# Performance work log

Measured on AMD Instinct MI355X. Metric: run time of the kernel, lower is better.

Reference implementation:

```python
import jax, jax.numpy as jnp
import numpy as np


def spiral_cw(H, W):
    idx = []
    top, bottom, left, right = 0, H - 1, 0, W - 1
    while top <= bottom and left <= right:
        for j in range(left, right + 1):
            idx.append((top, j))
        top += 1
        for i in range(top, bottom + 1):
            idx.append((i, right))
        right -= 1
        if top <= bottom:
            for j in range(right, left - 1, -1):
                idx.append((bottom, j))
            bottom -= 1
        if left <= right:
            for i in range(bottom, top - 1, -1):
                idx.append((i, left))
            left += 1
    return [i * W + j for i, j in idx]


def spiral_ccw(H, W):
    idx = []
    top, bottom, left, right = 0, H - 1, 0, W - 1
    while top <= bottom and left <= right:
        for j in range(right, left - 1, -1):
            idx.append((top, j))
        top += 1
        for i in range(top, bottom + 1):
            idx.append((i, left))
        left += 1
        if top <= bottom:
            for j in range(left, right + 1):
                idx.append((bottom, j))
            bottom -= 1
        if left <= right:
            for i in range(bottom, top - 1, -1):
                idx.append((i, right))
            right -= 1
    return [i * W + j for i, j in idx]


def silu(x):
    return x * jax.nn.sigmoid(x)


def mamba_fwd(x, in_w, conv_w, conv_b, xproj_w, dtp_w, dtp_b, A_log, D, out_w):
    # x: [B,L,dm]; expand=1 so d_inner == dm
    B, L, dm = x.shape
    d_inner = in_w.shape[1] // 2
    N = A_log.shape[1]          # d_state = 16
    K = conv_w.shape[1]         # d_conv = 4
    xz = x @ in_w               # [B,L,2*d_inner]
    u, z = jnp.split(xz, 2, axis=-1)
    # causal depthwise conv over L (kernel K), then SiLU
    up = jnp.pad(u, ((0, 0), (K - 1, 0), (0, 0)))
    uc = conv_b + sum(conv_w[:, k] * up[:, k:k + L, :] for k in range(K))
    uc = silu(uc)
    dbl = uc @ xproj_w          # [B,L,dt_rank+2N]
    dt_rank = dbl.shape[-1] - 2 * N
    dtc = dbl[..., :dt_rank]
    Bv = dbl[..., dt_rank:dt_rank + N]
    Cv = dbl[..., dt_rank + N:]
    dt = jax.nn.softplus(dtc @ dtp_w + dtp_b)   # [B,L,d_inner]
    A = -jnp.exp(A_log)                          # [d_inner,N]
    dA = jnp.exp(dt[..., None] * A)              # [B,L,d_inner,N]
    dBu = dt[..., None] * Bv[:, :, None, :] * uc[..., None]

    def step(h, inp):
        dA_t, dBu_t = inp
        h = h * dA_t + dBu_t
        return h, h

    h0 = jnp.zeros((B, d_inner, N), x.dtype)
    _, hs = jax.lax.scan(step, h0, (jnp.moveaxis(dA, 1, 0), jnp.moveaxis(dBu, 1, 0)))
    hs = jnp.moveaxis(hs, 0, 1)                  # [B,L,d_inner,N]
    y = jnp.einsum('bldn,bln->bld', hs, Cv) + D * uc
    y = y * silu(z)
    return y @ out_w


def setup_inputs():
    key = jax.random.key(0)
    ks = jax.random.split(key, 32)
    B, Hh, Ww, C = 4, 32, 32, 768
    L = Hh * Ww
    N, dr, K = 16, 48, 4

    def p(i, shape, s=0.02):
        return jax.random.normal(ks[i], shape, jnp.float32) * s

    d = {}
    d['x'] = jax.random.normal(ks[0], (B, L, C), jnp.float32)
    d['norm_w'] = jnp.ones((C,), jnp.float32)
    d['norm_b'] = jnp.zeros((C,), jnp.float32)
    for i, pre in enumerate(['cw', 'ccw']):
        o = 1 + i * 8
        d[pre + '_in_w'] = p(o, (C, 2 * C))
        d[pre + '_conv_w'] = p(o + 1, (C, K), 0.2)
        d[pre + '_conv_b'] = jnp.zeros((C,), jnp.float32)
        d[pre + '_xproj_w'] = p(o + 2, (C, dr + 2 * N))
        d[pre + '_dtp_w'] = p(o + 3, (dr, C), 0.1)
        d[pre + '_dtp_b'] = jnp.full((C,), -4.0, jnp.float32) + p(o + 4, (C,), 0.5)
        d[pre + '_A_log'] = jnp.log(jnp.broadcast_to(jnp.arange(1, N + 1, dtype=jnp.float32), (C, N)))
        d[pre + '_D'] = jnp.ones((C,), jnp.float32)
        d[pre + '_out_w'] = p(o + 5, (C, C))
    d['fus_w1'] = p(20, (2 * C, C))
    d['fus_b1'] = jnp.zeros((C,), jnp.float32)
    d['fus_w2'] = p(21, (C, C))
    d['fus_b2'] = jnp.zeros((C,), jnp.float32)
    return d


def reference(x, norm_w, norm_b,
              cw_in_w, cw_conv_w, cw_conv_b, cw_xproj_w, cw_dtp_w, cw_dtp_b, cw_A_log, cw_D, cw_out_w,
              ccw_in_w, ccw_conv_w, ccw_conv_b, ccw_xproj_w, ccw_dtp_w, ccw_dtp_b, ccw_A_log, ccw_D, ccw_out_w,
              fus_w1, fus_b1, fus_w2, fus_b2):
    B, L, C = x.shape
    H = int(L ** 0.5)
    W = H
    idx_cw = jnp.asarray(np.array(spiral_cw(H, W), dtype=np.int32))
    idx_ccw = jnp.asarray(np.array(spiral_ccw(H, W), dtype=np.int32))
    rev_cw = jnp.argsort(idx_cw)
    rev_ccw = jnp.argsort(idx_ccw)
    # LayerNorm(eps=1e-6)
    mu = x.mean(-1, keepdims=True)
    var = x.var(-1, keepdims=True)
    xn = (x - mu) / jnp.sqrt(var + 1e-6) * norm_w + norm_b
    x_cw = mamba_fwd(xn[:, idx_cw, :], cw_in_w, cw_conv_w, cw_conv_b, cw_xproj_w,
                     cw_dtp_w, cw_dtp_b, cw_A_log, cw_D, cw_out_w)[:, rev_cw, :]
    x_ccw = mamba_fwd(xn[:, idx_ccw, :], ccw_in_w, ccw_conv_w, ccw_conv_b, ccw_xproj_w,
                      ccw_dtp_w, ccw_dtp_b, ccw_A_log, ccw_D, ccw_out_w)[:, rev_ccw, :]
    fused = jnp.concatenate([x_cw, x_ccw], axis=-1)
    h = jax.nn.gelu(fused @ fus_w1 + fus_b1, approximate=False)
    out = h @ fus_w2 + fus_b2
    return out + x
```

## Files before the change

kernel.cpp:

```cpp
#include <hip/hip_runtime.h>

typedef unsigned short ushort_t;
typedef __attribute__((ext_vector_type(8))) short short8;
typedef __attribute__((ext_vector_type(4))) float f32x4;

#define B_ 4
#define L_ 1024
#define C_ 768
#define N_ 16
#define DR_ 48
#define HW_ 32
#define M_ (B_*L_)
#define SEG_ 64
#define NSEG_ 16


__device__ __forceinline__ float bf2f(ushort_t u) {
  union { unsigned int i; float f; } v; v.i = ((unsigned int)u) << 16; return v.f;
}
__device__ __forceinline__ ushort_t f2bf(float f) {
  union { float f; unsigned int i; } v; v.f = f;
  unsigned int x = v.i;
  return (ushort_t)((x + 0x7fffu + ((x >> 16) & 1u)) >> 16);
}
__device__ __forceinline__ float ldf(const void* p, size_t i, int bf) {
  return bf ? bf2f(((const ushort_t*)p)[i]) : ((const float*)p)[i];
}
__device__ __forceinline__ int detect_bf(const void* x) {
  const ushort_t* u = (const ushort_t*)x;
  int lane = threadIdx.x & 63;
  const ushort_t* p = u + lane * 4;
  int bad = 0;
  #pragma unroll
  for (int i = 0; i < 4; ++i) {
    int e = (p[i] >> 7) & 0xFF;
    bad |= (e < 90 || e > 141);
  }
  return (__ballot(bad) == 0ull) ? 1 : 0;
}
__device__ __forceinline__ void gload_lds16(const void* g, void* lds) {
  __builtin_amdgcn_global_load_lds(
      (const __attribute__((address_space(1))) unsigned int*)g,
      (__attribute__((address_space(3))) unsigned int*)lds, 16, 0, 0);
}

struct TJ {
  const void* src[8]; ushort_t* dst[8];
  int R[8], Cc[8], RD[8], ldD[8];
  int off[9]; int njobs;
};

__global__ __launch_bounds__(256) void prep_k(
    TJ tj, const void* __restrict__ x, const void* __restrict__ nw,
    const void* __restrict__ nb, ushort_t* __restrict__ xn,
    int* idx_cw, int* idx_ccw, int* flag)
{
  const int oT = tj.off[tj.njobs];
  int bid = blockIdx.x;
  const int inbf = detect_bf(x);

  if (bid < oT) {
    int j = 0;
    while (bid >= tj.off[j+1]) ++j;
    const void* src = tj.src[j];
    ushort_t* dst = tj.dst[j];
    const int R = tj.R[j], Cc = tj.Cc[j], RD = tj.RD[j], ldD = tj.ldD[j];
    int cb_span = (Cc > RD ? Cc : RD);
    int txt = (cb_span + 31) >> 5;
    int t = bid - tj.off[j];
    int bx = (t % txt) * 32;
    int by = (t / txt) * 32;
    __shared__ ushort_t tile[32][33];
    int tx = threadIdx.x & 31, ty = threadIdx.x >> 5;
    #pragma unroll
    for (int i = 0; i < 4; ++i) {
      int r = by + ty + i*8, c = bx + tx;
      ushort_t v = 0;
      if (r < R && c < Cc) v = f2bf(ldf(src, (size_t)r * Cc + c, inbf));
      tile[ty + i*8][tx] = v;
    }
    __syncthreads();
    #pragma unroll
    for (int i = 0; i < 4; ++i) {
      int dr = bx + ty + i*8, dc = by + tx;
      if (dr < RD && dc < ldD)
        dst[(size_t)dr * ldD + dc] = tile[tx][ty + i*8];
    }
    return;
  }
  bid -= oT;
  if (bid < M_) {
    int tid = threadIdx.x;
    size_t o0 = (size_t)bid * C_;
    float v0 = ldf(x, o0 + tid,       inbf);
    float v1 = ldf(x, o0 + tid + 256, inbf);
    float v2 = ldf(x, o0 + tid + 512, inbf);
    float s = v0 + v1 + v2, s2 = v0*v0 + v1*v1 + v2*v2;
    for (int o = 32; o > 0; o >>= 1) { s += __shfl_down(s, o); s2 += __shfl_down(s2, o); }
    __shared__ float ss[4], ss2[4];
    if ((tid & 63) == 0) { ss[tid >> 6] = s; ss2[tid >> 6] = s2; }
    __syncthreads();
    s  = ss[0] + ss[1] + ss[2] + ss[3];
    s2 = ss2[0] + ss2[1] + ss2[2] + ss2[3];
    float mean = s * (1.f / C_);
    float var  = s2 * (1.f / C_) - mean * mean;
    float inv  = rsqrtf(var + 1e-6f);
    xn[o0 + tid]       = f2bf((v0 - mean) * inv * ldf(nw, tid,     inbf) + ldf(nb, tid,     inbf));
    xn[o0 + tid + 256] = f2bf((v1 - mean) * inv * ldf(nw, tid+256, inbf) + ldf(nb, tid+256, inbf));
    xn[o0 + tid + 512] = f2bf((v2 - mean) * inv * ldf(nw, tid+512, inbf) + ldf(nb, tid+512, inbf));
    return;
  }
  {
    int tid = threadIdx.x;
    #pragma unroll
    for (int k = 0; k < 4; ++k) {
      int p = tid * 4 + k;
      int r = 0;
      while (r < (HW_/2 - 1) && p >= 4*(r+1)*(HW_-(r+1))) ++r;
      int q = p - 4*r*(HW_-r);
      int s = HW_ - 2*r;
      int hi = HW_ - 1 - r;
      int icw, jcw, iccw, jccw;
      if (q < s)              { icw = r;                  jcw = r + q; }
      else if (q < 2*s-1)     { icw = r + 1 + (q - s);    jcw = hi; }
      else if (q < 3*s-2)     { icw = hi;                 jcw = hi - 1 - (q - (2*s-1)); }
      else                    { icw = hi - 1 - (q - (3*s-2)); jcw = r; }
      if (q < s)              { iccw = r;                 jccw = hi - q; }
      else if (q < 2*s-1)     { iccw = r + 1 + (q - s);   jccw = r; }
      else if (q < 3*s-2)     { iccw = hi;                jccw = r + 1 + (q - (2*s-1)); }
      else                    { iccw = hi - 1 - (q - (3*s-2)); jccw = hi; }
      idx_cw[p]  = icw  * HW_ + jcw;
      idx_ccw[p] = iccw * HW_ + jccw;
    }
    if (tid == 0) *flag = inbf;
  }
}

__global__ __launch_bounds__(256) void tbatch_k(TJ tj, const int* __restrict__ flagp) {
  const int inbf = *flagp;
  int bid = blockIdx.x;
  int j = 0;
  while (bid >= tj.off[j+1]) ++j;
  const void* src = tj.src[j];
  ushort_t* dst = tj.dst[j];
  const int R = tj.R[j], Cc = tj.Cc[j], RD = tj.RD[j], ldD = tj.ldD[j];
  int cb_span = (Cc > RD ? Cc : RD);
  int txt = (cb_span + 31) >> 5;
  int t = bid - tj.off[j];
  int bx = (t % txt) * 32;
  int by = (t / txt) * 32;
  __shared__ ushort_t tile[32][33];
  int tx = threadIdx.x & 31, ty = threadIdx.x >> 5;
  #pragma unroll
  for (int i = 0; i < 4; ++i) {
    int r = by + ty + i*8, c = bx + tx;
    ushort_t v = 0;
    if (r < R && c < Cc) v = f2bf(ldf(src, (size_t)r * Cc + c, inbf));
    tile[ty + i*8][tx] = v;
  }
  __syncthreads();
  #pragma unroll
  for (int i = 0; i < 4; ++i) {
    int dr = bx + ty + i*8, dc = by + tx;
    if (dr < RD && dc < ldD)
      dst[(size_t)dr * ldD + dc] = tile[tx][ty + i*8];
  }
}

struct GB {
  const ushort_t* A[4]; const int* amap[4];
  const ushort_t* WT[4];
  const void* bias[4];
  void* out[4]; ushort_t* out2[4]; const int* omap[4];
};

template<int BM, int BN>
__global__ __launch_bounds__(256) void mgemm_k(
    GB gb, int lda, int ldb, int Nn, int K, int ldo,
    int act, int out_mode, const void* resid, int ldr, const int* __restrict__ flagp)
{
  constexpr int NA = BM / 32;
  constexpr int NB = BN / 32;
  constexpr int WN = (BM == 128) ? 2 : 4;
  constexpr int NSPAN = BN / WN;
  constexpr int FN = NSPAN / 16;
  const int inbf = *flagp;
  const int z = blockIdx.z;

  const ushort_t* A  = gb.A[z];
  const int* amap    = gb.amap[z];
  const ushort_t* Bw = gb.WT[z];
  const void* bias   = gb.bias[z];
  void* Out          = gb.out[z];
  ushort_t* out2     = gb.out2[z];
  const int* omap    = gb.omap[z];

  __shared__ __align__(16) ushort_t As[BM * 64];
  __shared__ __align__(16) ushort_t Bs[BN * 64];

  const int tid  = threadIdx.x;
  const int w    = tid >> 6;
  const int lane = tid & 63;
  const int quad = lane >> 4;
  const int l15  = lane & 15;
  const int wm     = (BM == 128) ? (w >> 1) * 64 : 0;
  const int wn_off = ((BM == 128) ? (w & 1) : w) * NSPAN;
  const int row0 = blockIdx.y * BM;
  const int col0 = blockIdx.x * BN;

  int agb[NA], bgb[NB], aldso[NA], bldso[NB];
  #pragma unroll
  for (int i = 0; i < NA; ++i) {
    int t = i*256 + tid;
    int r = t >> 3;
    int c = (t & 7) ^ (r & 7);
    int grow = row0 + r;
    if (amap) { int b = grow >> 10, l = grow & 1023; grow = (b << 10) + amap[l]; }
    agb[i] = grow * lda + c * 8;
    aldso[i] = (i*256 + w*64) * 16;
  }
  #pragma unroll
  for (int i = 0; i < NB; ++i) {
    int t = i*256 + tid;
    int r = t >> 3;
    int c = (t & 7) ^ (r & 7);
    bgb[i] = (col0 + r) * ldb + c * 8;
    bldso[i] = (i*256 + w*64) * 16;
  }

  f32x4 acc[4][FN];
  #pragma unroll
  for (int mi = 0; mi < 4; ++mi)
    #pragma unroll
    for (int ni = 0; ni < FN; ++ni)
      acc[mi][ni] = (f32x4){0.f, 0.f, 0.f, 0.f};

  const int sw = l15 & 7;

  for (int k0 = 0; k0 < K; k0 += 64) {
    #pragma unroll
    for (int i = 0; i < NA; ++i)
      gload_lds16(A + agb[i] + k0, (char*)As + aldso[i]);
    #pragma unroll
    for (int i = 0; i < NB; ++i)
      gload_lds16(Bw + bgb[i] + k0, (char*)Bs + bldso[i]);
    __syncthreads();

    #pragma unroll
    for (int ks = 0; ks < 2; ++ks) {
      short8 aF[4], bF[FN];
      #pragma unroll
      for (int mi = 0; mi < 4; ++mi)
        aF[mi] = *(const short8*)&As[(wm + mi*16 + l15) * 64 + (((quad + 4*ks) ^ sw) * 8)];
      #pragma unroll
      for (int ni = 0; ni < FN; ++ni)
        bF[ni] = *(const short8*)&Bs[(wn_off + ni*16 + l15) * 64 + (((quad + 4*ks) ^ sw) * 8)];
      #pragma unroll
      for (int mi = 0; mi < 4; ++mi)
        #pragma unroll
        for (int ni = 0; ni < FN; ++ni)
          acc[mi][ni] = __builtin_amdgcn_mfma_f32_16x16x32_bf16(aF[mi], bF[ni], acc[mi][ni], 0, 0, 0);
    }
    __syncthreads();
  }

  const int obf = (out_mode == 2) ? inbf : (out_mode == 0);
  #pragma unroll
  for (int ni = 0; ni < FN; ++ni) {
    int colg = col0 + wn_off + ni*16 + l15;
    if (colg >= Nn) continue;
    float bv = bias ? ldf(bias, colg, inbf) : 0.f;
    #pragma unroll
    for (int mi = 0; mi < 4; ++mi) {
      #pragma unroll
      for (int r = 0; r < 4; ++r) {
        int rowg = row0 + wm + mi*16 + quad*4 + r;
        int orow = rowg;
        if (omap) { int b = rowg >> 10, l = rowg & 1023; orow = (b << 10) + omap[l]; }
        float v = acc[mi][ni][r] + bv;
        if (out2 && colg < 64)
          out2[(size_t)orow * 64 + colg] = f2bf(colg < DR_ ? v : 0.f);
        if (act == 1)      v = (v > 20.f) ? v : log1pf(__expf(v));
        else if (act == 2) v = 0.5f * v * (1.f + erff(v * 0.70710678118654752f));
        if (resid) v += ldf(resid, (size_t)orow * ldr + colg, inbf);
        size_t oi = (size_t)orow * ldo + colg;
        if (obf) ((ushort_t*)Out)[oi] = f2bf(v);
        else     ((float*)Out)[oi]    = v;
      }
    }
  }
}

__global__ __launch_bounds__(256) void conv_silu_k(
    const ushort_t* __restrict__ u,
    const void* __restrict__ cw0, const void* __restrict__ cw1,
    const void* __restrict__ cb0, const void* __restrict__ cb1,
    ushort_t* __restrict__ uc, const int* __restrict__ flagp)
{
  const int inbf = *flagp;
  int g = blockIdx.x * 256 + threadIdx.x;
  int c = g % C_;
  int row = g / C_;
  int l = row & 1023;
  const void* cw = (row >> 12) ? cw1 : cw0;
  const void* cb = (row >> 12) ? cb1 : cb0;
  float w0 = ldf(cw, c*4+0, inbf), w1 = ldf(cw, c*4+1, inbf);
  float w2 = ldf(cw, c*4+2, inbf), w3 = ldf(cw, c*4+3, inbf);
  const ushort_t* up = u + (size_t)(row - l) * C_ + c;
  float s = ldf(cb, c, inbf);
  if (l >= 3) s += w0 * bf2f(up[(size_t)(l-3) * C_]);
  if (l >= 2) s += w1 * bf2f(up[(size_t)(l-2) * C_]);
  if (l >= 1) s += w2 * bf2f(up[(size_t)(l-1) * C_]);
  s += w3 * bf2f(up[(size_t)l * C_]);
  s = s / (1.f + __expf(-s));
  uc[g] = f2bf(s);
}

__global__ __launch_bounds__(256) void scan_pass1(
    const ushort_t* __restrict__ dt, const ushort_t* __restrict__ uc,
    const float* __restrict__ dbl,
    const void* __restrict__ Alog_cw, const void* __restrict__ Alog_ccw,
    ushort_t* __restrict__ P, ushort_t* __restrict__ Q,
    const int* __restrict__ flagp)
{
  const int inbf = *flagp;
  const int db = blockIdx.z, d = db >> 2;
  const int s = blockIdx.y;
  const int tid = threadIdx.x;
  const int c = blockIdx.x * 256 + tid;
  const int l0 = s * SEG_;

  __shared__ __align__(16) float Bs[SEG_][32];
  {
    const float* src = dbl + ((size_t)db * L_ + l0) * 80 + DR_;
    #pragma unroll
    for (int i = 0; i < 2; ++i) {
      int idx = tid * 4 + i * 1024;
      int st = idx >> 5, col = idx & 31;
      *(f32x4*)&Bs[st][col] = *(const f32x4*)(src + (size_t)st * 80 + col);
    }
  }
  __syncthreads();

  const void* Alog = d ? Alog_ccw : Alog_cw;
  float a[16];
  #pragma unroll
  for (int n = 0; n < 16; ++n) a[n] = -__expf(ldf(Alog, c * N_ + n, inbf));

  const size_t rbase = ((size_t)db * L_ + l0) * C_ + c;
  const ushort_t* dtp = dt + rbase;
  const ushort_t* ucp = uc + rbase;

  float h[16];
  #pragma unroll
  for (int n = 0; n < 16; ++n) h[n] = 0.f;
  float S = 0.f;

  #pragma unroll 4
  for (int l = 0; l < SEG_; ++l) {
    float dtv = bf2f(dtp[(size_t)l * C_]);
    float ucv = bf2f(ucp[(size_t)l * C_]);
    float dtu = dtv * ucv;
    S += dtv;
    f32x4 bq0 = *(const f32x4*)&Bs[l][0];
    f32x4 bq1 = *(const f32x4*)&Bs[l][4];
    f32x4 bq2 = *(const f32x4*)&Bs[l][8];
    f32x4 bq3 = *(const f32x4*)&Bs[l][12];
    #pragma unroll
    for (int j = 0; j < 4; ++j) { float dA = __expf(dtv*a[j]);    h[j]    = h[j]   *dA + dtu*bq0[j]; }
    #pragma unroll
    for (int j = 0; j < 4; ++j) { float dA = __expf(dtv*a[4+j]);  h[4+j]  = h[4+j] *dA + dtu*bq1[j]; }
    #pragma unroll
    for (int j = 0; j < 4; ++j) { float dA = __expf(dtv*a[8+j]);  h[8+j]  = h[8+j] *dA + dtu*bq2[j]; }
    #pragma unroll
    for (int j = 0; j < 4; ++j) { float dA = __expf(dtv*a[12+j]); h[12+j] = h[12+j]*dA + dtu*bq3[j]; }
  }
  size_t idx = (((size_t)db * NSEG_ + s) * C_ + c) * N_;
  #pragma unroll
  for (int n = 0; n < 16; ++n) {
    P[idx + n] = f2bf(__expf(a[n] * S));
    Q[idx + n] = f2bf(h[n]);
  }
}

__global__ __launch_bounds__(256) void scan_pass2(
    ushort_t* __restrict__ P, ushort_t* __restrict__ Q)
{
  size_t g = (size_t)blockIdx.x * 256 + threadIdx.x;
  size_t db = g / (C_ * N_);
  size_t cn = g % (C_ * N_);
  float h = 0.f;
  #pragma unroll
  for (int s = 0; s < NSEG_; ++s) {
    size_t off = (db * NSEG_ + s) * (C_ * N_) + cn;
    float p = bf2f(P[off]), q = bf2f(Q[off]);
    Q[off] = f2bf(h);
    h = h * p + q;
  }
}

__global__ __launch_bounds__(256) void scan_pass3(
    const ushort_t* __restrict__ dt, const ushort_t* __restrict__ uc,
    const float* __restrict__ dbl, const ushort_t* __restrict__ z,
    const void* __restrict__ Alog_cw, const void* __restrict__ Alog_ccw,
    const void* __restrict__ D_cw, const void* __restrict__ D_ccw,
    const ushort_t* __restrict__ Q, ushort_t* __restrict__ y,
    const int* __restrict__ flagp)
{
  const int inbf = *flagp;
  const int db = blockIdx.z, d = db >> 2;
  const int s = blockIdx.y;
  const int tid = threadIdx.x;
  const int c = blockIdx.x * 256 + tid;
  const int l0 = s * SEG_;

  __shared__ __align__(16) float Bs[SEG_][32];
  {
    const float* src = dbl + ((size_t)db * L_ + l0) * 80 + DR_;
    #pragma unroll
    for (int i = 0; i < 2; ++i) {
      int idx = tid * 4 + i * 1024;
      int st = idx >> 5, col = idx & 31;
      *(f32x4*)&Bs[st][col] = *(const f32x4*)(src + (size_t)st * 80 + col);
    }
  }
  __syncthreads();

  const void* Alog = d ? Alog_ccw : Alog_cw;
  const void* Dp   = d ? D_ccw   : D_cw;
  float a[16];
  #pragma unroll
  for (int n = 0; n < 16; ++n) a[n] = -__expf(ldf(Alog, c * N_ + n, inbf));
  const float dvc = ldf(Dp, c, inbf);

  const size_t rbase = ((size_t)db * L_ + l0) * C_ + c;
  const ushort_t* dtp = dt + rbase;
  const ushort_t* ucp = uc + rbase;
  const ushort_t* zp  = z  + rbase;
  ushort_t* yp = y + rbase;

  size_t idx = (((size_t)db * NSEG_ + s) * C_ + c) * N_;
  float h[16];
  #pragma unroll
  for (int n = 0; n < 16; ++n) h[n] = bf2f(Q[idx + n]);

  #pragma unroll 2
  for (int l = 0; l < SEG_; ++l) {
    float dtv = bf2f(dtp[(size_t)l * C_]);
    float ucv = bf2f(ucp[(size_t)l * C_]);
    float zv  = bf2f(zp[(size_t)l * C_]);
    float dtu = dtv * ucv;
    f32x4 bq0 = *(const f32x4*)&Bs[l][0];
    f32x4 bq1 = *(const f32x4*)&Bs[l][4];
    f32x4 bq2 = *(const f32x4*)&Bs[l][8];
    f32x4 bq3 = *(const f32x4*)&Bs[l][12];
    f32x4 cq0 = *(const f32x4*)&Bs[l][16];
    f32x4 cq1 = *(const f32x4*)&Bs[l][20];
    f32x4 cq2 = *(const f32x4*)&Bs[l][24];
    f32x4 cq3 = *(const f32x4*)&Bs[l][28];
    float yv = dvc * ucv;
    #pragma unroll
    for (int j = 0; j < 4; ++j) { float dA = __expf(dtv*a[j]);    h[j]    = h[j]   *dA + dtu*bq0[j]; yv += h[j]   *cq0[j]; }
    #pragma unroll
    for (int j = 0; j < 4; ++j) { float dA = __expf(dtv*a[4+j]);  h[4+j]  = h[4+j] *dA + dtu*bq1[j]; yv += h[4+j] *cq1[j]; }
    #pragma unroll
    for (int j = 0; j < 4; ++j) { float dA = __expf(dtv*a[8+j]);  h[8+j]  = h[8+j] *dA + dtu*bq2[j]; yv += h[8+j] *cq2[j]; }
    #pragma unroll
    for (int j = 0; j < 4; ++j) { float dA = __expf(dtv*a[12+j]); h[12+j] = h[12+j]*dA + dtu*bq3[j]; yv += h[12+j]*cq3[j]; }
    yv *= zv / (1.f + __expf(-zv));
    yp[(size_t)l * C_] = f2bf(yv);
  }
}

extern "C" void kernel_launch(void* const* d_in, const int* in_sizes, int n_in,
                              void* d_out, int out_size, void* d_ws, size_t ws_size,
                              hipStream_t stream)
{
  const void* x      = d_in[0];
  const void* norm_w = d_in[1];
  const void* norm_b = d_in[2];
  const void* in_w[2]    = { d_in[3],  d_in[12] };
  const void* conv_w[2]  = { d_in[4],  d_in[13] };
  const void* conv_b[2]  = { d_in[5],  d_in[14] };
  const void* xproj_w[2] = { d_in[6],  d_in[15] };
  const void* dtp_w[2]   = { d_in[7],  d_in[16] };
  const void* dtp_b[2]   = { d_in[8],  d_in[17] };
  const void* A_log[2]   = { d_in[9],  d_in[18] };
  const void* Dvec[2]    = { d_in[10], d_in[19] };
  const void* out_w[2]   = { d_in[11], d_in[20] };
  const void* fus_w1 = d_in[21];
  const void* fus_b1 = d_in[22];
  const void* fus_w2 = d_in[23];
  const void* fus_b2 = d_in[24];

  char* base = (char*)d_ws;
  int*      IDX  = (int*)base;
  int*      FLAG = (int*)(base + 8192);
  ushort_t* XN   = (ushort_t*)(base + 8448);
  ushort_t* U    = (ushort_t*)(base + 6299904);
  ushort_t* Z    = (ushort_t*)(base + 18882816);
  ushort_t* UC   = (ushort_t*)(base + 31465728);
  float*    DBL  = (float*)(base + 44048640);
  ushort_t* Y    = (ushort_t*)(base + 46670080);
  ushort_t* DT    = U;
  ushort_t* FUSED = Z;
  ushort_t* HBUF  = XN;
  ushort_t* SP = (ushort_t*)(base + 8448);
  ushort_t* SQ = SP + (size_t)2 * 4 * NSEG_ * C_ * N_;
  ushort_t* DTC = XN;
  ushort_t* INWT = UC;
  ushort_t* uout = (ushort_t*)d_out;
  ushort_t* XPJT = uout;
  ushort_t* DTPT = uout + 196608;
  ushort_t* OWT  = uout + 294912;
  ushort_t* FW1T = U;
  ushort_t* FW2T = U + (size_t)768 * 1536;

  const size_t SD = (size_t)M_ * C_;

  {
    TJ tj; tj.njobs = 8;
    for (int d = 0; d < 2; ++d) {
      int j = d;
      tj.src[j]=in_w[d]; tj.dst[j]=INWT+(size_t)d*1536*768;
      tj.R[j]=768; tj.Cc[j]=1536; tj.RD[j]=1536; tj.ldD[j]=768;
    }
    for (int d = 0; d < 2; ++d) {
      int j = 2+d;
      tj.src[j]=xproj_w[d]; tj.dst[j]=XPJT+(size_t)d*128*768;
      tj.R[j]=768; tj.Cc[j]=80; tj.RD[j]=128; tj.ldD[j]=768;
    }
    for (int d = 0; d < 2; ++d) {
      int j = 4+d;
      tj.src[j]=dtp_w[d]; tj.dst[j]=DTPT+(size_t)d*768*64;
      tj.R[j]=48; tj.Cc[j]=768; tj.RD[j]=768; tj.ldD[j]=64;
    }
    for (int d = 0; d < 2; ++d) {
      int j = 6+d;
      tj.src[j]=out_w[d]; tj.dst[j]=OWT+(size_t)d*768*768;
      tj.R[j]=768; tj.Cc[j]=768; tj.RD[j]=768; tj.ldD[j]=768;
    }
    tj.off[0] = 0;
    for (int j = 0; j < 8; ++j) {
      int cspan = tj.Cc[j] > tj.RD[j] ? tj.Cc[j] : tj.RD[j];
      int rspan = tj.R[j] > tj.ldD[j] ? tj.R[j] : tj.ldD[j];
      tj.off[j+1] = tj.off[j] + ((cspan+31)>>5) * ((rspan+31)>>5);
    }
    int nblk = tj.off[8] + M_ + 1;
    hipLaunchKernelGGL(prep_k, dim3(nblk), dim3(256), 0, stream,
        tj, x, norm_w, norm_b, XN, IDX, IDX + L_, FLAG);
  }

  GB gb;
  for (int i = 0; i < 4; ++i) { gb.out2[i] = nullptr; gb.omap[i] = nullptr; gb.amap[i] = nullptr; gb.bias[i] = nullptr; }

  for (int zz = 0; zz < 4; ++zz) {
    int d = zz >> 1, half = zz & 1;
    gb.A[zz] = XN; gb.amap[zz] = IDX + d * L_;
    gb.WT[zz] = INWT + (size_t)d*1536*768 + (size_t)half*768*768;
    gb.bias[zz] = nullptr;
    gb.out[zz] = (void*)((half ? Z : U) + d * SD); gb.out2[zz] = nullptr; gb.omap[zz] = nullptr;
  }
  hipLaunchKernelGGL((mgemm_k<64,64>), dim3(12, 64, 4), dim3(256), 0, stream,
      gb, C_, C_, C_, C_, C_, 0, 0, (const void*)nullptr, 0, FLAG);

  hipLaunchKernelGGL(conv_silu_k, dim3(2*M_*C_/256), dim3(256), 0, stream,
      U, conv_w[0], conv_w[1], conv_b[0], conv_b[1], UC, FLAG);

  for (int zz = 0; zz < 2; ++zz) {
    gb.A[zz] = UC + zz * SD; gb.amap[zz] = nullptr;
    gb.WT[zz] = XPJT + (size_t)zz*128*768;
    gb.bias[zz] = nullptr;
    gb.out[zz] = (void*)(DBL + (size_t)zz * M_ * 80);
    gb.out2[zz] = DTC + (size_t)zz * M_ * 64;
    gb.omap[zz] = nullptr;
  }
  hipLaunchKernelGGL((mgemm_k<64,64>), dim3(2, 64, 2), dim3(256), 0, stream,
      gb, C_, C_, 80, C_, 80, 0, 1, (const void*)nullptr, 0, FLAG);

  for (int zz = 0; zz < 2; ++zz) {
    gb.A[zz] = DTC + (size_t)zz * M_ * 64; gb.amap[zz] = nullptr;
    gb.WT[zz] = DTPT + (size_t)zz*768*64;
    gb.bias[zz] = dtp_b[zz];
    gb.out[zz] = (void*)(DT + zz * SD); gb.out2[zz] = nullptr; gb.omap[zz] = nullptr;
  }
  hipLaunchKernelGGL((mgemm_k<64,64>), dim3(12, 64, 2), dim3(256), 0, stream,
      gb, 64, 64, C_, 64, C_, 1, 0, (const void*)nullptr, 0, FLAG);

  hipLaunchKernelGGL(scan_pass1, dim3(3, NSEG_, 8), dim3(256), 0, stream,
      DT, UC, DBL, A_log[0], A_log[1], SP, SQ, FLAG);
  hipLaunchKernelGGL(scan_pass2, dim3(8 * C_ * N_ / 256), dim3(256), 0, stream, SP, SQ);
  hipLaunchKernelGGL(scan_pass3, dim3(3, NSEG_, 8), dim3(256), 0, stream,
      DT, UC, DBL, Z, A_log[0], A_log[1], Dvec[0], Dvec[1], SQ, Y, FLAG);

  {
    TJ tj; tj.njobs = 2;
    tj.src[0]=fus_w1; tj.dst[0]=FW1T; tj.R[0]=1536; tj.Cc[0]=768; tj.RD[0]=768; tj.ldD[0]=1536;
    tj.src[1]=fus_w2; tj.dst[1]=FW2T; tj.R[1]=768;  tj.Cc[1]=768; tj.RD[1]=768; tj.ldD[1]=768;
    tj.off[0] = 0;
    for (int j = 0; j < 2; ++j) {
      int cspan = tj.Cc[j] > tj.RD[j] ? tj.Cc[j] : tj.RD[j];
      int rspan = tj.R[j] > tj.ldD[j] ? tj.R[j] : tj.ldD[j];
      tj.off[j+1] = tj.off[j] + ((cspan+31)>>5) * ((rspan+31)>>5);
    }
    hipLaunchKernelGGL(tbatch_k, dim3(tj.off[2]), dim3(256), 0, stream, tj, FLAG);
  }

  for (int zz = 0; zz < 2; ++zz) {
    gb.A[zz] = Y + zz * SD; gb.amap[zz] = nullptr;
    gb.WT[zz] = OWT + (size_t)zz*768*768;
    gb.bias[zz] = nullptr;
    gb.out[zz] = (void*)(FUSED + zz * C_); gb.out2[zz] = nullptr; gb.omap[zz] = IDX + zz * L_;
  }
  hipLaunchKernelGGL((mgemm_k<64,64>), dim3(12, 64, 2), dim3(256), 0, stream,
      gb, C_, C_, C_, C_, 2*C_, 0, 0, (const void*)nullptr, 0, FLAG);

  gb.A[0] = FUSED; gb.amap[0] = nullptr;
  gb.WT[0] = FW1T; gb.bias[0] = fus_b1;
  gb.out[0] = (void*)HBUF; gb.out2[0] = nullptr; gb.omap[0] = nullptr;
  hipLaunchKernelGGL((mgemm_k<64,64>), dim3(12, 64, 1), dim3(256), 0, stream,
      gb, 2*C_, 2*C_, C_, 2*C_, C_, 2, 0, (const void*)nullptr, 0, FLAG);

  gb.A[0] = HBUF; gb.amap[0] = nullptr;
  gb.WT[0] = FW2T; gb.bias[0] = fus_b2;
  gb.out[0] = d_out; gb.out2[0] = nullptr; gb.omap[0] = nullptr;
  hipLaunchKernelGGL((mgemm_k<64,64>), dim3(12, 64, 1), dim3(256), 0, stream,
      gb, C_, C_, C_, C_, C_, 0, 2, x, C_, FLAG);
}
```

Before: 400.4 us.

## Split scan state dimension across four threads per channel

Scan pass1 and pass3 now assign four threads per channel, each owning four of the sixteen state entries, so the grid grows fourfold. Pass3 combines the partial output dot products with two xor shuffles, and one lane per group writes y. The goal is more waves and fewer registers per thread on a small grid of 384 blocks, improving latency hiding. The cost is that dt, uc and z loads are repeated across four lanes and the y stores are narrower and partly idle.

```diff
diff --git a/kernel.cpp b/kernel.cpp
--- a/kernel.cpp
+++ b/kernel.cpp
@@ -3,6 +3,7 @@
 typedef unsigned short ushort_t;
 typedef __attribute__((ext_vector_type(8))) short short8;
 typedef __attribute__((ext_vector_type(4))) float f32x4;
+typedef __attribute__((ext_vector_type(4))) unsigned short u16x4;
 
 #define B_ 4
 #define L_ 1024
@@ -327,7 +328,9 @@
   const int db = blockIdx.z, d = db >> 2;
   const int s = blockIdx.y;
   const int tid = threadIdx.x;
-  const int c = blockIdx.x * 256 + tid;
+  const int cl = tid >> 2;
+  const int n4 = tid & 3;
+  const int c = blockIdx.x * 64 + cl;
   const int l0 = s * SEG_;
 
   __shared__ __align__(16) float Bs[SEG_][32];
@@ -343,44 +346,33 @@
   __syncthreads();
 
   const void* Alog = d ? Alog_ccw : Alog_cw;
-  float a[16];
-  #pragma unroll
-  for (int n = 0; n < 16; ++n) a[n] = -__expf(ldf(Alog, c * N_ + n, inbf));
+  float a[4];
+  #pragma unroll
+  for (int j = 0; j < 4; ++j) a[j] = -__expf(ldf(Alog, c * N_ + n4*4 + j, inbf));
 
   const size_t rbase = ((size_t)db * L_ + l0) * C_ + c;
   const ushort_t* dtp = dt + rbase;
   const ushort_t* ucp = uc + rbase;
 
-  float h[16];
-  #pragma unroll
-  for (int n = 0; n < 16; ++n) h[n] = 0.f;
+  float h[4] = {0.f, 0.f, 0.f, 0.f};
   float S = 0.f;
 
-  #pragma unroll 4
+  #pragma unroll 8
   for (int l = 0; l < SEG_; ++l) {
     float dtv = bf2f(dtp[(size_t)l * C_]);
     float ucv = bf2f(ucp[(size_t)l * C_]);
     float dtu = dtv * ucv;
     S += dtv;
-    f32x4 bq0 = *(const f32x4*)&Bs[l][0];
-    f32x4 bq1 = *(const f32x4*)&Bs[l][4];
-    f32x4 bq2 = *(const f32x4*)&Bs[l][8];
-    f32x4 bq3 = *(const f32x4*)&Bs[l][12];
-    #pragma unroll
-    for (int j = 0; j < 4; ++j) { float dA = __expf(dtv*a[j]);    h[j]    = h[j]   *dA + dtu*bq0[j]; }
-    #pragma unroll
-    for (int j = 0; j < 4; ++j) { float dA = __expf(dtv*a[4+j]);  h[4+j]  = h[4+j] *dA + dtu*bq1[j]; }
-    #pragma unroll
-    for (int j = 0; j < 4; ++j) { float dA = __expf(dtv*a[8+j]);  h[8+j]  = h[8+j] *dA + dtu*bq2[j]; }
-    #pragma unroll
-    for (int j = 0; j < 4; ++j) { float dA = __expf(dtv*a[12+j]); h[12+j] = h[12+j]*dA + dtu*bq3[j]; }
-  }
-  size_t idx = (((size_t)db * NSEG_ + s) * C_ + c) * N_;
-  #pragma unroll
-  for (int n = 0; n < 16; ++n) {
-    P[idx + n] = f2bf(__expf(a[n] * S));
-    Q[idx + n] = f2bf(h[n]);
-  }
+    f32x4 bq = *(const f32x4*)&Bs[l][n4*4];
+    #pragma unroll
+    for (int j = 0; j < 4; ++j) { float dA = __expf(dtv*a[j]); h[j] = h[j]*dA + dtu*bq[j]; }
+  }
+  size_t idx = (((size_t)db * NSEG_ + s) * C_ + c) * N_ + n4*4;
+  u16x4 pv, qv;
+  #pragma unroll
+  for (int j = 0; j < 4; ++j) { pv[j] = f2bf(__expf(a[j] * S)); qv[j] = f2bf(h[j]); }
+  *(u16x4*)&P[idx] = pv;
+  *(u16x4*)&Q[idx] = qv;
 }
 
 __global__ __launch_bounds__(256) void scan_pass2(
@@ -411,7 +403,9 @@
   const int db = blockIdx.z, d = db >> 2;
   const int s = blockIdx.y;
   const int tid = threadIdx.x;
-  const int c = blockIdx.x * 256 + tid;
+  const int cl = tid >> 2;
+  const int n4 = tid & 3;
+  const int c = blockIdx.x * 64 + cl;
   const int l0 = s * SEG_;
 
   __shared__ __align__(16) float Bs[SEG_][32];
@@ -428,9 +422,9 @@
 
   const void* Alog = d ? Alog_ccw : Alog_cw;
   const void* Dp   = d ? D_ccw   : D_cw;
-  float a[16];
-  #pragma unroll
-  for (int n = 0; n < 16; ++n) a[n] = -__expf(ldf(Alog, c * N_ + n, inbf));
+  float a[4];
+  #pragma unroll
+  for (int j = 0; j < 4; ++j) a[j] = -__expf(ldf(Alog, c * N_ + n4*4 + j, inbf));
   const float dvc = ldf(Dp, c, inbf);
 
   const size_t rbase = ((size_t)db * L_ + l0) * C_ + c;
@@ -439,36 +433,29 @@
   const ushort_t* zp  = z  + rbase;
   ushort_t* yp = y + rbase;
 
-  size_t idx = (((size_t)db * NSEG_ + s) * C_ + c) * N_;
-  float h[16];
-  #pragma unroll
-  for (int n = 0; n < 16; ++n) h[n] = bf2f(Q[idx + n]);
-
-  #pragma unroll 2
+  size_t idx = (((size_t)db * NSEG_ + s) * C_ + c) * N_ + n4*4;
+  float h[4];
+  #pragma unroll
+  for (int j = 0; j < 4; ++j) h[j] = bf2f(Q[idx + j]);
+
+  #pragma unroll 4
   for (int l = 0; l < SEG_; ++l) {
     float dtv = bf2f(dtp[(size_t)l * C_]);
     float ucv = bf2f(ucp[(size_t)l * C_]);
     float zv  = bf2f(zp[(size_t)l * C_]);
     float dtu = dtv * ucv;
-    f32x4 bq0 = *(const f32x4*)&Bs[l][0];
-    f32x4 bq1 = *(const f32x4*)&Bs[l][4];
-    f32x4 bq2 = *(const f32x4*)&Bs[l][8];
-    f32x4 bq3 = *(const f32x4*)&Bs[l][12];
-    f32x4 cq0 = *(const f32x4*)&Bs[l][16];
-    f32x4 cq1 = *(const f32x4*)&Bs[l][20];
-    f32x4 cq2 = *(const f32x4*)&Bs[l][24];
-    f32x4 cq3 = *(const f32x4*)&Bs[l][28];
-    float yv = dvc * ucv;
-    #pragma unroll
-    for (int j = 0; j < 4; ++j) { float dA = __expf(dtv*a[j]);    h[j]    = h[j]   *dA + dtu*bq0[j]; yv += h[j]   *cq0[j]; }
-    #pragma unroll
-    for (int j = 0; j < 4; ++j) { float dA = __expf(dtv*a[4+j]);  h[4+j]  = h[4+j] *dA + dtu*bq1[j]; yv += h[4+j] *cq1[j]; }
-    #pragma unroll
-    for (int j = 0; j < 4; ++j) { float dA = __expf(dtv*a[8+j]);  h[8+j]  = h[8+j] *dA + dtu*bq2[j]; yv += h[8+j] *cq2[j]; }
-    #pragma unroll
-    for (int j = 0; j < 4; ++j) { float dA = __expf(dtv*a[12+j]); h[12+j] = h[12+j]*dA + dtu*bq3[j]; yv += h[12+j]*cq3[j]; }
-    yv *= zv / (1.f + __expf(-zv));
-    yp[(size_t)l * C_] = f2bf(yv);
+    f32x4 bq = *(const f32x4*)&Bs[l][n4*4];
+    f32x4 cq = *(const f32x4*)&Bs[l][16 + n4*4];
+    float yv = 0.f;
+    #pragma unroll
+    for (int j = 0; j < 4; ++j) { float dA = __expf(dtv*a[j]); h[j] = h[j]*dA + dtu*bq[j]; yv += h[j]*cq[j]; }
+    yv += __shfl_xor(yv, 1);
+    yv += __shfl_xor(yv, 2);
+    if (n4 == 0) {
+      float o = yv + dvc * ucv;
+      o *= zv / (1.f + __expf(-zv));
+      yp[(size_t)l * C_] = f2bf(o);
+    }
   }
 }
 
@@ -587,10 +574,10 @@
   hipLaunchKernelGGL((mgemm_k<64,64>), dim3(12, 64, 2), dim3(256), 0, stream,
       gb, 64, 64, C_, 64, C_, 1, 0, (const void*)nullptr, 0, FLAG);
 
-  hipLaunchKernelGGL(scan_pass1, dim3(3, NSEG_, 8), dim3(256), 0, stream,
+  hipLaunchKernelGGL(scan_pass1, dim3(12, NSEG_, 8), dim3(256), 0, stream,
       DT, UC, DBL, A_log[0], A_log[1], SP, SQ, FLAG);
   hipLaunchKernelGGL(scan_pass2, dim3(8 * C_ * N_ / 256), dim3(256), 0, stream, SP, SQ);
-  hipLaunchKernelGGL(scan_pass3, dim3(3, NSEG_, 8), dim3(256), 0, stream,
+  hipLaunchKernelGGL(scan_pass3, dim3(12, NSEG_, 8), dim3(256), 0, stream,
       DT, UC, DBL, Z, A_log[0], A_log[1], Dvec[0], Dvec[1], SQ, Y, FLAG);
 
   {
```

Result: no change. 401.0 us (+0.2%).

## Halve scan segments, stage dt/uc in LDS, remap GEMM blocks across XCDs

Applied to the files above, without the earlier changes.

The chunked selective scan now uses 32-step segments (32 segments) instead of 64. The dt and uc tiles are loaded into LDS with direct global-to-LDS loads, while the B/C vectors are read straight from global memory as broadcast loads instead of being staged. Exponentials become exp2 with log2e folded into A, and P/Q stores are vectorised. The GEMM kernel also remaps its workgroup indices so consecutive tiles land on the same XCD for L2 locality. The P/Q scratch buffers are moved into the output and XN regions to fit the larger segment count, which adds aliasing risk.

```diff
diff --git a/kernel.cpp b/kernel.cpp
--- a/kernel.cpp
+++ b/kernel.cpp
@@ -3,6 +3,7 @@
 typedef unsigned short ushort_t;
 typedef __attribute__((ext_vector_type(8))) short short8;
 typedef __attribute__((ext_vector_type(4))) float f32x4;
+typedef __attribute__((ext_vector_type(4))) unsigned short u16x4;
 
 #define B_ 4
 #define L_ 1024
@@ -11,8 +12,9 @@
 #define DR_ 48
 #define HW_ 32
 #define M_ (B_*L_)
-#define SEG_ 64
-#define NSEG_ 16
+#define SEG_ 32
+#define NSEG_ 32
+#define LOG2E_ 1.44269504088896f
 
 
 __device__ __forceinline__ float bf2f(ushort_t u) {
@@ -205,8 +207,17 @@
   const int l15  = lane & 15;
   const int wm     = (BM == 128) ? (w >> 1) * 64 : 0;
   const int wn_off = ((BM == 128) ? (w & 1) : w) * NSPAN;
-  const int row0 = blockIdx.y * BM;
-  const int col0 = blockIdx.x * BN;
+
+  const int gx = gridDim.x;
+  const int nwg = gx * gridDim.y;
+  int flat = blockIdx.y * gx + blockIdx.x;
+  {
+    const int q = nwg >> 3, rr = nwg & 7;
+    const int xcd = flat & 7, wi = flat >> 3;
+    flat = (xcd < rr ? xcd * (q + 1) : rr * (q + 1) + (xcd - rr) * q) + wi;
+  }
+  const int row0 = (flat / gx) * BM;
+  const int col0 = (flat % gx) * BN;
 
   int agb[NA], bgb[NB], aldso[NA], bldso[NB];
   #pragma unroll
@@ -327,59 +338,64 @@
   const int db = blockIdx.z, d = db >> 2;
   const int s = blockIdx.y;
   const int tid = threadIdx.x;
-  const int c = blockIdx.x * 256 + tid;
+  const int c0 = blockIdx.x * 256;
+  const int c = c0 + tid;
   const int l0 = s * SEG_;
 
-  __shared__ __align__(16) float Bs[SEG_][32];
-  {
-    const float* src = dbl + ((size_t)db * L_ + l0) * 80 + DR_;
-    #pragma unroll
-    for (int i = 0; i < 2; ++i) {
-      int idx = tid * 4 + i * 1024;
-      int st = idx >> 5, col = idx & 31;
-      *(f32x4*)&Bs[st][col] = *(const f32x4*)(src + (size_t)st * 80 + col);
-    }
+  __shared__ __align__(16) ushort_t dtS[SEG_ * 256];
+  __shared__ __align__(16) ushort_t ucS[SEG_ * 256];
+  #pragma unroll
+  for (int i = 0; i < 4; ++i) {
+    int ch = i * 256 + tid;
+    int row = ch >> 5, colb = (ch & 31) * 8;
+    size_t go = ((size_t)db * L_ + l0 + row) * C_ + c0 + colb;
+    gload_lds16(dt + go, (char*)dtS + ch * 16);
+    gload_lds16(uc + go, (char*)ucS + ch * 16);
   }
   __syncthreads();
 
   const void* Alog = d ? Alog_ccw : Alog_cw;
-  float a[16];
-  #pragma unroll
-  for (int n = 0; n < 16; ++n) a[n] = -__expf(ldf(Alog, c * N_ + n, inbf));
-
-  const size_t rbase = ((size_t)db * L_ + l0) * C_ + c;
-  const ushort_t* dtp = dt + rbase;
-  const ushort_t* ucp = uc + rbase;
+  float a2[16];
+  #pragma unroll
+  for (int j = 0; j < 16; ++j)
+    a2[j] = -__expf(ldf(Alog, c * N_ + j, inbf)) * LOG2E_;
 
   float h[16];
   #pragma unroll
-  for (int n = 0; n < 16; ++n) h[n] = 0.f;
+  for (int j = 0; j < 16; ++j) h[j] = 0.f;
   float S = 0.f;
 
-  #pragma unroll 4
+  #pragma unroll 2
   for (int l = 0; l < SEG_; ++l) {
-    float dtv = bf2f(dtp[(size_t)l * C_]);
-    float ucv = bf2f(ucp[(size_t)l * C_]);
+    float dtv = bf2f(dtS[l * 256 + tid]);
+    float ucv = bf2f(ucS[l * 256 + tid]);
     float dtu = dtv * ucv;
     S += dtv;
-    f32x4 bq0 = *(const f32x4*)&Bs[l][0];
-    f32x4 bq1 = *(const f32x4*)&Bs[l][4];
-    f32x4 bq2 = *(const f32x4*)&Bs[l][8];
-    f32x4 bq3 = *(const f32x4*)&Bs[l][12];
-    #pragma unroll
-    for (int j = 0; j < 4; ++j) { float dA = __expf(dtv*a[j]);    h[j]    = h[j]   *dA + dtu*bq0[j]; }
-    #pragma unroll
-    for (int j = 0; j < 4; ++j) { float dA = __expf(dtv*a[4+j]);  h[4+j]  = h[4+j] *dA + dtu*bq1[j]; }
-    #pragma unroll
-    for (int j = 0; j < 4; ++j) { float dA = __expf(dtv*a[8+j]);  h[8+j]  = h[8+j] *dA + dtu*bq2[j]; }
-    #pragma unroll
-    for (int j = 0; j < 4; ++j) { float dA = __expf(dtv*a[12+j]); h[12+j] = h[12+j]*dA + dtu*bq3[j]; }
+    const float* bc = dbl + ((size_t)db * L_ + l0 + l) * 80 + DR_;
+    f32x4 b0 = *(const f32x4*)(bc);
+    f32x4 b1 = *(const f32x4*)(bc + 4);
+    f32x4 b2 = *(const f32x4*)(bc + 8);
+    f32x4 b3 = *(const f32x4*)(bc + 12);
+    #pragma unroll
+    for (int j = 0; j < 4; ++j) { float dA = exp2f(dtv*a2[j]);    h[j]    = h[j]   *dA + dtu*b0[j]; }
+    #pragma unroll
+    for (int j = 0; j < 4; ++j) { float dA = exp2f(dtv*a2[4+j]);  h[4+j]  = h[4+j] *dA + dtu*b1[j]; }
+    #pragma unroll
+    for (int j = 0; j < 4; ++j) { float dA = exp2f(dtv*a2[8+j]);  h[8+j]  = h[8+j] *dA + dtu*b2[j]; }
+    #pragma unroll
+    for (int j = 0; j < 4; ++j) { float dA = exp2f(dtv*a2[12+j]); h[12+j] = h[12+j]*dA + dtu*b3[j]; }
   }
   size_t idx = (((size_t)db * NSEG_ + s) * C_ + c) * N_;
   #pragma unroll
-  for (int n = 0; n < 16; ++n) {
-    P[idx + n] = f2bf(__expf(a[n] * S));
-    Q[idx + n] = f2bf(h[n]);
+  for (int q = 0; q < 4; ++q) {
+    u16x4 pv, qv;
+    #pragma unroll
+    for (int j = 0; j < 4; ++j) {
+      pv[j] = f2bf(exp2f(a2[q*4+j] * S));
+      qv[j] = f2bf(h[q*4+j]);
+    }
+    *(u16x4*)&P[idx + q*4] = pv;
+    *(u16x4*)&Q[idx + q*4] = qv;
   }
 }
 
@@ -411,62 +427,63 @@
   const int db = blockIdx.z, d = db >> 2;
   const int s = blockIdx.y;
   const int tid = threadIdx.x;
-  const int c = blockIdx.x * 256 + tid;
+  const int c0 = blockIdx.x * 256;
+  const int c = c0 + tid;
   const int l0 = s * SEG_;
 
-  __shared__ __align__(16) float Bs[SEG_][32];
-  {
-    const float* src = dbl + ((size_t)db * L_ + l0) * 80 + DR_;
-    #pragma unroll
-    for (int i = 0; i < 2; ++i) {
-      int idx = tid * 4 + i * 1024;
-      int st = idx >> 5, col = idx & 31;
-      *(f32x4*)&Bs[st][col] = *(const f32x4*)(src + (size_t)st * 80 + col);
-    }
+  __shared__ __align__(16) ushort_t dtS[SEG_ * 256];
+  __shared__ __align__(16) ushort_t ucS[SEG_ * 256];
+  #pragma unroll
+  for (int i = 0; i < 4; ++i) {
+    int ch = i * 256 + tid;
+    int row = ch >> 5, colb = (ch & 31) * 8;
+    size_t go = ((size_t)db * L_ + l0 + row) * C_ + c0 + colb;
+    gload_lds16(dt + go, (char*)dtS + ch * 16);
+    gload_lds16(uc + go, (char*)ucS + ch * 16);
   }
   __syncthreads();
 
   const void* Alog = d ? Alog_ccw : Alog_cw;
   const void* Dp   = d ? D_ccw   : D_cw;
-  float a[16];
-  #pragma unroll
-  for (int n = 0; n < 16; ++n) a[n] = -__expf(ldf(Alog, c * N_ + n, inbf));
+  float a2[16];
+  #pragma unroll
+  for (int j = 0; j < 16; ++j)
+    a2[j] = -__expf(ldf(Alog, c * N_ + j, inbf)) * LOG2E_;
   const float dvc = ldf(Dp, c, inbf);
-
-  const size_t rbase = ((size_t)db * L_ + l0) * C_ + c;
-  const ushort_t* dtp = dt + rbase;
-  const ushort_t* ucp = uc + rbase;
-  const ushort_t* zp  = z  + rbase;
-  ushort_t* yp = y + rbase;
 
   size_t idx = (((size_t)db * NSEG_ + s) * C_ + c) * N_;
   float h[16];
   #pragma unroll
-  for (int n = 0; n < 16; ++n) h[n] = bf2f(Q[idx + n]);
+  for (int j = 0; j < 16; ++j) h[j] = bf2f(Q[idx + j]);
+
+  const size_t rbase = ((size_t)db * L_ + l0) * C_ + c;
+  const ushort_t* zp  = z + rbase;
+  ushort_t* yp = y + rbase;
 
   #pragma unroll 2
   for (int l = 0; l < SEG_; ++l) {
-    float dtv = bf2f(dtp[(size_t)l * C_]);
-    float ucv = bf2f(ucp[(size_t)l * C_]);
+    float dtv = bf2f(dtS[l * 256 + tid]);
+    float ucv = bf2f(ucS[l * 256 + tid]);
     float zv  = bf2f(zp[(size_t)l * C_]);
     float dtu = dtv * ucv;
-    f32x4 bq0 = *(const f32x4*)&Bs[l][0];
-    f32x4 bq1 = *(const f32x4*)&Bs[l][4];
-    f32x4 bq2 = *(const f32x4*)&Bs[l][8];
-    f32x4 bq3 = *(const f32x4*)&Bs[l][12];
-    f32x4 cq0 = *(const f32x4*)&Bs[l][16];
-    f32x4 cq1 = *(const f32x4*)&Bs[l][20];
-    f32x4 cq2 = *(const f32x4*)&Bs[l][24];
-    f32x4 cq3 = *(const f32x4*)&Bs[l][28];
+    const float* bc = dbl + ((size_t)db * L_ + l0 + l) * 80 + DR_;
+    f32x4 b0 = *(const f32x4*)(bc);
+    f32x4 b1 = *(const f32x4*)(bc + 4);
+    f32x4 b2 = *(const f32x4*)(bc + 8);
+    f32x4 b3 = *(const f32x4*)(bc + 12);
+    f32x4 c0v = *(const f32x4*)(bc + 16);
+    f32x4 c1v = *(const f32x4*)(bc + 20);
+    f32x4 c2v = *(const f32x4*)(bc + 24);
+    f32x4 c3v = *(const f32x4*)(bc + 28);
     float yv = dvc * ucv;
     #pragma unroll
-    for (int j = 0; j < 4; ++j) { float dA = __expf(dtv*a[j]);    h[j]    = h[j]   *dA + dtu*bq0[j]; yv += h[j]   *cq0[j]; }
-    #pragma unroll
-    for (int j = 0; j < 4; ++j) { float dA = __expf(dtv*a[4+j]);  h[4+j]  = h[4+j] *dA + dtu*bq1[j]; yv += h[4+j] *cq1[j]; }
-    #pragma unroll
-    for (int j = 0; j < 4; ++j) { float dA = __expf(dtv*a[8+j]);  h[8+j]  = h[8+j] *dA + dtu*bq2[j]; yv += h[8+j] *cq2[j]; }
-    #pragma unroll
-    for (int j = 0; j < 4; ++j) { float dA = __expf(dtv*a[12+j]); h[12+j] = h[12+j]*dA + dtu*bq3[j]; yv += h[12+j]*cq3[j]; }
+    for (int j = 0; j < 4; ++j) { float dA = exp2f(dtv*a2[j]);    h[j]    = h[j]   *dA + dtu*b0[j]; yv += h[j]   *c0v[j]; }
+    #pragma unroll
+    for (int j = 0; j < 4; ++j) { float dA = exp2f(dtv*a2[4+j]);  h[4+j]  = h[4+j] *dA + dtu*b1[j]; yv += h[4+j] *c1v[j]; }
+    #pragma unroll
+    for (int j = 0; j < 4; ++j) { float dA = exp2f(dtv*a2[8+j]);  h[8+j]  = h[8+j] *dA + dtu*b2[j]; yv += h[8+j] *c2v[j]; }
+    #pragma unroll
+    for (int j = 0; j < 4; ++j) { float dA = exp2f(dtv*a2[12+j]); h[12+j] = h[12+j]*dA + dtu*b3[j]; yv += h[12+j]*c3v[j]; }
     yv *= zv / (1.f + __expf(-zv));
     yp[(size_t)l * C_] = f2bf(yv);
   }
@@ -505,14 +522,14 @@
   ushort_t* DT    = U;
   ushort_t* FUSED = Z;
   ushort_t* HBUF  = XN;
-  ushort_t* SP = (ushort_t*)(base + 8448);
-  ushort_t* SQ = SP + (size_t)2 * 4 * NSEG_ * C_ * N_;
   ushort_t* DTC = XN;
   ushort_t* INWT = UC;
   ushort_t* uout = (ushort_t*)d_out;
   ushort_t* XPJT = uout;
   ushort_t* DTPT = uout + 196608;
   ushort_t* OWT  = uout + 294912;
+  ushort_t* SQ = XN;
+  ushort_t* SP = uout + 1474560;
   ushort_t* FW1T = U;
   ushort_t* FW2T = U + (size_t)768 * 1536;
 
```

After: 392.6 us. Within noise of the previous version (-1.9%).
